# Performance work log

Measured on AMD Instinct MI355X. Metric: run time of the kernel, lower is better.

The kernel has to match this reference:

```python
import jax, jax.numpy as jnp
import numpy as np

N = 8192
STATE_DIM = 64
HIDDENS = [512, 512]
LATENT = 128
TEMP = 1.0
EPS = 1e-12  # torch F.normalize eps


def _linear_params(key, fan_in, fan_out):
    k1, k2 = jax.random.split(key)
    bound = 1.0 / np.sqrt(fan_in)
    W = jax.random.uniform(k1, (fan_in, fan_out), jnp.float32, -bound, bound)
    b = jax.random.uniform(k2, (fan_out,), jnp.float32, -bound, bound)
    return W, b


def setup_inputs() -> dict:
    key = jax.random.key(0)
    ks = jax.random.split(key, 6)
    x = jax.random.normal(ks[0], (N, STATE_DIM), jnp.float32)
    y = jax.random.normal(ks[1], (N, STATE_DIM), jnp.float32)
    # state encoder params (forward uses state_enc for both x and y, as in source)
    W1, b1 = _linear_params(ks[2], STATE_DIM, HIDDENS[0])
    W2, b2 = _linear_params(ks[3], HIDDENS[0], HIDDENS[1])
    W3, b3 = _linear_params(ks[4], HIDDENS[1], LATENT)
    return {"x": x, "y": y, "W1": W1, "b1": b1, "W2": W2, "b2": b2, "W3": W3, "b3": b3}


def _encode(h, W1, b1, W2, b2, W3, b3):
    h = jax.nn.relu(h @ W1 + b1)
    h = jax.nn.relu(h @ W2 + b2)
    return h @ W3 + b3


def _l2norm(z):
    # matches torch F.normalize(dim=-1): z / max(||z||, eps)
    n = jnp.sqrt(jnp.sum(z * z, axis=-1, keepdims=True))
    return z / jnp.maximum(n, EPS)


def reference(x, y, W1, b1, W2, b2, W3, b3):
    zx = _l2norm(_encode(x, W1, b1, W2, b2, W3, b3))  # [N, LATENT]
    zy = _l2norm(_encode(y, W1, b1, W2, b2, W3, b3))  # [N, LATENT]
    # sum(x[:,None,:]*y[None,:,:], -1) == zx @ zy.T, expressed as tiled GEMM
    return jnp.einsum('id,jd->ij', zx, zy) / TEMP  # [N, N]
```

## Files before the change

kernel.cpp:

```cpp
#include <hip/hip_runtime.h>
#include <hip/hip_bf16.h>
#include <cstdint>
#include <cstddef>


typedef unsigned short u16;
typedef __attribute__((ext_vector_type(8))) short bf16x8;
typedef __attribute__((ext_vector_type(4))) float f32x4;

__device__ __forceinline__ u16 f_to_bf16_bits(float f) {
    union { float f; uint32_t u; } v; v.f = f;
    uint32_t lsb = (v.u >> 16) & 1u;
    return (u16)((v.u + 0x7fffu + lsb) >> 16);
}

__global__ __launch_bounds__(256) void cast_f32_bf16_kernel(
    const float* __restrict__ in, u16* __restrict__ out, int n)
{
    int i = blockIdx.x * 256 + threadIdx.x;
    if (i < n) out[i] = f_to_bf16_bits(in[i]);
}

__global__ __launch_bounds__(256) void transpose_cast_kernel(
    const float* __restrict__ in, u16* __restrict__ out, int R, int C)
{
    int idx = blockIdx.x * 256 + threadIdx.x;
    if (idx < R * C) {
        int r = idx / C, c = idx - r * C;
        out[c * R + r] = f_to_bf16_bits(in[r * C + c]);
    }
}

template<bool RELU, bool BIAS, bool OUT_F32>
__global__ __launch_bounds__(256) void gemm_bt_kernel(
    const u16* __restrict__ A, const u16* __restrict__ BT,
    const float* __restrict__ bias,
    u16* __restrict__ Cb, float* __restrict__ Cf,
    int M, int N, int K)
{
    const int lane = threadIdx.x & 63;
    const int wave = threadIdx.x >> 6;
    const int wm = wave >> 1, wn = wave & 1;
    const int m_base = blockIdx.y * 128 + wm * 64;
    const int n_base = blockIdx.x * 128 + wn * 64;
    const int mi   = lane & 15;
    const int quad = lane >> 4;

    f32x4 acc[4][4];
    #pragma unroll
    for (int i = 0; i < 4; ++i)
        #pragma unroll
        for (int j = 0; j < 4; ++j)
            acc[i][j] = f32x4{0.f, 0.f, 0.f, 0.f};

    const u16* arow[4];
    const u16* brow[4];
    #pragma unroll
    for (int i = 0; i < 4; ++i)
        arow[i] = A + (size_t)(m_base + i * 16 + mi) * K + quad * 8;
    #pragma unroll
    for (int j = 0; j < 4; ++j)
        brow[j] = BT + (size_t)(n_base + j * 16 + mi) * K + quad * 8;

    for (int k0 = 0; k0 < K; k0 += 32) {
        bf16x8 af[4], bfr[4];
        #pragma unroll
        for (int i = 0; i < 4; ++i)
            af[i] = *reinterpret_cast<const bf16x8*>(arow[i] + k0);
        #pragma unroll
        for (int j = 0; j < 4; ++j)
            bfr[j] = *reinterpret_cast<const bf16x8*>(brow[j] + k0);
        #pragma unroll
        for (int i = 0; i < 4; ++i)
            #pragma unroll
            for (int j = 0; j < 4; ++j)
                acc[i][j] = __builtin_amdgcn_mfma_f32_16x16x32_bf16(
                    af[i], bfr[j], acc[i][j], 0, 0, 0);
    }

    #pragma unroll
    for (int j = 0; j < 4; ++j) {
        const int col = n_base + j * 16 + mi;
        float bv = BIAS ? bias[col] : 0.f;
        #pragma unroll
        for (int i = 0; i < 4; ++i) {
            const int row0 = m_base + i * 16 + quad * 4;
            #pragma unroll
            for (int r = 0; r < 4; ++r) {
                float v = acc[i][j][r] + bv;
                if (RELU) v = fmaxf(v, 0.f);
                if (OUT_F32) Cf[(size_t)(row0 + r) * N + col] = v;
                else         Cb[(size_t)(row0 + r) * N + col] = f_to_bf16_bits(v);
            }
        }
    }
}

__global__ __launch_bounds__(256) void l2norm_kernel(
    const float* __restrict__ z, u16* __restrict__ zn)
{
    const int row  = blockIdx.x * 4 + (threadIdx.x >> 6);
    const int lane = threadIdx.x & 63;
    const float2* zp = reinterpret_cast<const float2*>(z + (size_t)row * 128);
    float2 p = zp[lane];
    float s = p.x * p.x + p.y * p.y;
    #pragma unroll
    for (int off = 32; off > 0; off >>= 1)
        s += __shfl_xor(s, off, 64);
    float inv = 1.0f / fmaxf(sqrtf(s), 1e-12f);
    uint32_t outp = (uint32_t)f_to_bf16_bits(p.x * inv)
                  | ((uint32_t)f_to_bf16_bits(p.y * inv) << 16);
    reinterpret_cast<uint32_t*>(zn + (size_t)row * 128)[lane] = outp;
}

extern "C" void kernel_launch(void* const* d_in, const int* in_sizes, int n_in,
                              void* d_out, int out_size, void* d_ws, size_t ws_size,
                              hipStream_t stream)
{
    const float* x  = (const float*)d_in[0];
    const float* y  = (const float*)d_in[1];
    const float* W1 = (const float*)d_in[2];
    const float* b1 = (const float*)d_in[3];
    const float* W2 = (const float*)d_in[4];
    const float* b2 = (const float*)d_in[5];
    const float* W3 = (const float*)d_in[6];
    const float* b3 = (const float*)d_in[7];
    float* out = (float*)d_out;

    u16* ws  = (u16*)d_ws;
    u16* xy  = ws;
    u16* W1T = xy  + (size_t)16384 * 64;
    u16* W2T = W1T + 512 * 64;
    u16* W3T = W2T + 512 * 512;
    u16* h1  = W3T + 128 * 512;
    u16* h2  = h1  + (size_t)16384 * 512;
    u16* zn  = h2  + (size_t)16384 * 512;
    float* z = (float*)(zn + (size_t)16384 * 128);

    dim3 blk(256);

    cast_f32_bf16_kernel<<<(8192 * 64 + 255) / 256, blk, 0, stream>>>(
        x, xy, 8192 * 64);
    cast_f32_bf16_kernel<<<(8192 * 64 + 255) / 256, blk, 0, stream>>>(
        y, xy + (size_t)8192 * 64, 8192 * 64);

    transpose_cast_kernel<<<(64 * 512 + 255) / 256, blk, 0, stream>>>(W1, W1T, 64, 512);
    transpose_cast_kernel<<<(512 * 512 + 255) / 256, blk, 0, stream>>>(W2, W2T, 512, 512);
    transpose_cast_kernel<<<(512 * 128 + 255) / 256, blk, 0, stream>>>(W3, W3T, 512, 128);

    gemm_bt_kernel<true, true, false><<<dim3(4, 128), blk, 0, stream>>>(
        xy, W1T, b1, h1, nullptr, 16384, 512, 64);
    gemm_bt_kernel<true, true, false><<<dim3(4, 128), blk, 0, stream>>>(
        h1, W2T, b2, h2, nullptr, 16384, 512, 512);
    gemm_bt_kernel<false, true, true><<<dim3(1, 128), blk, 0, stream>>>(
        h2, W3T, b3, nullptr, z, 16384, 128, 512);

    l2norm_kernel<<<16384 / 4, blk, 0, stream>>>(z, zn);

    gemm_bt_kernel<false, false, true><<<dim3(64, 64), blk, 0, stream>>>(
        zn, zn + (size_t)8192 * 128, nullptr, nullptr, out, 8192, 8192, 128);
}
```

Before: 405.1 us.

## Stage GEMM operand tiles in LDS via direct global-to-LDS loads

The GEMM kernel is rewritten so the block cooperatively loads A and B tiles into shared memory using global_load_lds. Each wave then reads its fragments from LDS instead of issuing redundant global loads. Before, each wave loaded its own rows and the two waves sharing rows or columns duplicated those loads. This halves global traffic per block but adds two barriers per K-step with no double buffering, so load latency is no longer overlapped with compute. The final large GEMM is dominated by its output store, which may limit any benefit.

```diff
diff --git a/kernel.cpp b/kernel.cpp
--- a/kernel.cpp
+++ b/kernel.cpp
@@ -32,17 +32,18 @@
 }
 
 template<bool RELU, bool BIAS, bool OUT_F32>
-__global__ __launch_bounds__(256) void gemm_bt_kernel(
+__global__ __launch_bounds__(256) void gemm_lds_kernel(
     const u16* __restrict__ A, const u16* __restrict__ BT,
     const float* __restrict__ bias,
     u16* __restrict__ Cb, float* __restrict__ Cf,
     int M, int N, int K)
 {
+    __shared__ u16 lds[16 * 512];
     const int lane = threadIdx.x & 63;
     const int wave = threadIdx.x >> 6;
     const int wm = wave >> 1, wn = wave & 1;
-    const int m_base = blockIdx.y * 128 + wm * 64;
-    const int n_base = blockIdx.x * 128 + wn * 64;
+    const int m_base = blockIdx.y * 128;
+    const int n_base = blockIdx.x * 128;
     const int mi   = lane & 15;
     const int quad = lane >> 4;
 
@@ -53,38 +54,54 @@
         for (int j = 0; j < 4; ++j)
             acc[i][j] = f32x4{0.f, 0.f, 0.f, 0.f};
 
-    const u16* arow[4];
-    const u16* brow[4];
+    const u16* src[4];
     #pragma unroll
-    for (int i = 0; i < 4; ++i)
-        arow[i] = A + (size_t)(m_base + i * 16 + mi) * K + quad * 8;
-    #pragma unroll
-    for (int j = 0; j < 4; ++j)
-        brow[j] = BT + (size_t)(n_base + j * 16 + mi) * K + quad * 8;
+    for (int s = 0; s < 4; ++s) {
+        const int t = wave * 4 + s;
+        if (t < 8)
+            src[s] = A + (size_t)(m_base + t * 16 + mi) * K + quad * 8;
+        else
+            src[s] = BT + (size_t)(n_base + (t - 8) * 16 + mi) * K + quad * 8;
+    }
+    u16* dst_base = &lds[wave * 4 * 512];
 
     for (int k0 = 0; k0 < K; k0 += 32) {
+        #pragma unroll
+        for (int s = 0; s < 4; ++s) {
+            __builtin_amdgcn_global_load_lds(
+                (const __attribute__((address_space(1))) void*)(src[s] + k0),
+                (__attribute__((address_space(3))) void*)(dst_base + s * 512),
+                16, 0, 0);
+        }
+        __syncthreads();
+
         bf16x8 af[4], bfr[4];
         #pragma unroll
         for (int i = 0; i < 4; ++i)
-            af[i] = *reinterpret_cast<const bf16x8*>(arow[i] + k0);
+            af[i] = *reinterpret_cast<const bf16x8*>(&lds[(wm * 4 + i) * 512 + lane * 8]);
         #pragma unroll
         for (int j = 0; j < 4; ++j)
-            bfr[j] = *reinterpret_cast<const bf16x8*>(brow[j] + k0);
+            bfr[j] = *reinterpret_cast<const bf16x8*>(&lds[(8 + wn * 4 + j) * 512 + lane * 8]);
+
         #pragma unroll
         for (int i = 0; i < 4; ++i)
             #pragma unroll
             for (int j = 0; j < 4; ++j)
                 acc[i][j] = __builtin_amdgcn_mfma_f32_16x16x32_bf16(
                     af[i], bfr[j], acc[i][j], 0, 0, 0);
+
+        __syncthreads();
     }
 
+    const int wm_base = m_base + wm * 64;
+    const int wn_base = n_base + wn * 64;
     #pragma unroll
     for (int j = 0; j < 4; ++j) {
-        const int col = n_base + j * 16 + mi;
+        const int col = wn_base + j * 16 + mi;
         float bv = BIAS ? bias[col] : 0.f;
         #pragma unroll
         for (int i = 0; i < 4; ++i) {
-            const int row0 = m_base + i * 16 + quad * 4;
+            const int row0 = wm_base + i * 16 + quad * 4;
             #pragma unroll
             for (int r = 0; r < 4; ++r) {
                 float v = acc[i][j][r] + bv;
@@ -148,15 +165,15 @@
     transpose_cast_kernel<<<(512 * 512 + 255) / 256, blk, 0, stream>>>(W2, W2T, 512, 512);
     transpose_cast_kernel<<<(512 * 128 + 255) / 256, blk, 0, stream>>>(W3, W3T, 512, 128);
 
-    gemm_bt_kernel<true, true, false><<<dim3(4, 128), blk, 0, stream>>>(
+    gemm_lds_kernel<true, true, false><<<dim3(4, 128), blk, 0, stream>>>(
         xy, W1T, b1, h1, nullptr, 16384, 512, 64);
-    gemm_bt_kernel<true, true, false><<<dim3(4, 128), blk, 0, stream>>>(
+    gemm_lds_kernel<true, true, false><<<dim3(4, 128), blk, 0, stream>>>(
         h1, W2T, b2, h2, nullptr, 16384, 512, 512);
-    gemm_bt_kernel<false, true, true><<<dim3(1, 128), blk, 0, stream>>>(
+    gemm_lds_kernel<false, true, true><<<dim3(1, 128), blk, 0, stream>>>(
         h2, W3T, b3, nullptr, z, 16384, 128, 512);
 
     l2norm_kernel<<<16384 / 4, blk, 0, stream>>>(z, zn);
 
-    gemm_bt_kernel<false, false, true><<<dim3(64, 64), blk, 0, stream>>>(
+    gemm_lds_kernel<false, false, true><<<dim3(64, 64), blk, 0, stream>>>(
         zn, zn + (size_t)8192 * 128, nullptr, nullptr, out, 8192, 8192, 128);
 }
```

New measurement: 378.5 us. 1.07x faster.
